# Optimization experiments

Measured on AMD Instinct MI355X. Metric: run time of the kernel, lower is better.

## Reference

```python
import jax, jax.numpy as jnp
import numpy as np

BATCH = 1024
N_KPS = 24
N_IN = 6
N_HID = 128
N_OUT = 2
N_EDGES = N_KPS * (N_KPS - 1)  # 552, fully-connected minus self-loops
BN_EPS = 1e-5


def _xavier(key, shape):
    # torch xavier_normal_: std = sqrt(2 / (fan_in + fan_out)); Linear weight is [out, in]
    std = np.sqrt(2.0 / (shape[0] + shape[1])).astype(np.float32)
    return jax.random.normal(key, shape, dtype=jnp.float32) * std


def _mlp(x, w1, b1, w2, b2, g, be):
    # Two-layer ELU MLP followed by training-mode BatchNorm1d over flattened (B*N, C)
    h = jax.nn.elu(jnp.einsum('bnd,hd->bnh', x, w1) + b1)
    h = jax.nn.elu(jnp.einsum('bnd,hd->bnh', h, w2) + b2)
    mean = h.mean(axis=(0, 1))
    var = h.var(axis=(0, 1))  # biased variance, as torch BN uses for normalization
    return g * (h - mean) * jax.lax.rsqrt(var + BN_EPS) + be


def setup_inputs() -> dict:
    key = jax.random.key(0)
    ks = jax.random.split(key, 12)
    # structural one-hot receiver/sender matrices for fully-connected graph (no self-loops)
    off = ~np.eye(N_KPS, dtype=bool)
    recv_idx, send_idx = np.nonzero(off)
    eye = np.eye(N_KPS, dtype=np.float32)
    rel_rec = jnp.asarray(eye[recv_idx])    # [E, N]
    rel_send = jnp.asarray(eye[send_idx])   # [E, N]

    inputs = jax.random.normal(ks[0], (BATCH, N_KPS, N_IN), dtype=jnp.float32)

    def mlp_params(k, n_in):
        k1, k2 = jax.random.split(k)
        return dict(
            w1=_xavier(k1, (N_HID, n_in)), b1=jnp.full((N_HID,), 0.1, jnp.float32),
            w2=_xavier(k2, (N_HID, N_HID)), b2=jnp.full((N_HID,), 0.1, jnp.float32),
            g=jnp.ones((N_HID,), jnp.float32), be=jnp.zeros((N_HID,), jnp.float32))

    m1 = mlp_params(ks[1], N_IN)
    m2 = mlp_params(ks[2], 2 * N_HID)
    m3 = mlp_params(ks[3], N_HID)
    m4 = mlp_params(ks[4], 3 * N_HID)
    fo_w = _xavier(ks[5], (N_OUT, N_HID * N_KPS))
    fo_b = jnp.full((N_OUT,), 0.1, jnp.float32)

    d = {'inputs': inputs, 'rel_rec': rel_rec, 'rel_send': rel_send,
         'fo_w': fo_w, 'fo_b': fo_b}
    for name, p in [('m1', m1), ('m2', m2), ('m3', m3), ('m4', m4)]:
        for k2, v in p.items():
            d[f'{name}_{k2}'] = v
    return d


def reference(inputs, rel_rec, rel_send,
              fo_w, fo_b,
              m1_w1, m1_b1, m1_w2, m1_b2, m1_g, m1_be,
              m2_w1, m2_b1, m2_w2, m2_b2, m2_g, m2_be,
              m3_w1, m3_b1, m3_w2, m3_b2, m3_g, m3_be,
              m4_w1, m4_b1, m4_w2, m4_b2, m4_g, m4_be):
    B, N = inputs.shape[0], inputs.shape[1]
    x = inputs.reshape(B, N, -1)

    def node2edge(x):  # [B,N,C] -> [B,E,2C]
        recv = jnp.einsum('en,bnc->bec', rel_rec, x)
        send = jnp.einsum('en,bnc->bec', rel_send, x)
        return jnp.concatenate([recv, send], axis=2)

    def edge2node(x):  # [B,E,C] -> [B,N,C], averaged by N (= incoming.size(1))
        return jnp.einsum('en,bec->bnc', rel_rec, x) / N

    x = _mlp(x, m1_w1, m1_b1, m1_w2, m1_b2, m1_g, m1_be)            # [B,N,H]
    x = _mlp(node2edge(x), m2_w1, m2_b1, m2_w2, m2_b2, m2_g, m2_be)  # [B,E,H]
    x_skip = x
    x = _mlp(edge2node(x), m3_w1, m3_b1, m3_w2, m3_b2, m3_g, m3_be)  # [B,N,H]
    x = node2edge(x)                                                  # [B,E,2H]
    x = jnp.concatenate([x, x_skip], axis=2)                          # [B,E,3H]
    x = _mlp(x, m4_w1, m4_b1, m4_w2, m4_b2, m4_g, m4_be)              # [B,E,H]
    x = edge2node(x)                                                  # [B,N,H]
    x = x.reshape(B, -1)                                              # [B,N*H]
    return x @ fo_w.T + fo_b                                          # [B,n_out]
```

## Files before the change

### kernel.cpp

```cpp
#include <hip/hip_runtime.h>

typedef __bf16 bf16;
typedef __bf16 b16x8 __attribute__((ext_vector_type(8)));
typedef __bf16 b16x4 __attribute__((ext_vector_type(4)));
typedef float f32x4 __attribute__((ext_vector_type(4)));

#define TB 256
#define LDA 136
#define NB 1024
#define NK 24
#define NE 552
#define NH 128
#define BEcnt (NB*NE)
#define BNODE (NB*NK)
#define EPS 1e-5f

#define S_BN1 0
#define S_BN3 2048
#define S_A2  4096
#define S_A4  20480
#define S_SC2 36864
#define S_SC4 37120
#define S_B41 37376
#define STATS_ZERO_BYTES 147456
#define WB_M1W2 0
#define WB_M2W1 16384
#define WB_M2W2 49152
#define WB_M3W1 65536
#define WB_M3W2 81920
#define WB_M4W1 98304
#define WB_M4W2 147456
#define WB_M4W1S 163840
#define OFF_WBF 150528ull
#define OFF_H1  516096ull
#define OFF_H3  (OFF_H1 + 6291456ull)
#define OFF_Y2R (OFF_H3 + 6291456ull)
#define OFF_Y2S (OFF_Y2R + 6291456ull)
#define OFF_Y4R (OFF_Y2S + 6291456ull)
#define OFF_Y4S (OFF_Y4R + 6291456ull)
#define OFF_Z2  (OFF_Y4S + 6291456ull)
#define OFF_Z4  (OFF_Z2  + 12582912ull)
#define OFF_H2  (OFF_Z4  + 12582912ull)

__device__ __forceinline__ float elu(float x){ return x > 0.f ? x : __expf(x) - 1.f; }

__device__ __forceinline__ void swizzle_bt(int id, int& b, int& tile4){
  int x = id & 7, j = id >> 3;
  int bt = j / 6;
  int tile = j - bt*6;
  b = x*128 + bt;
  tile4 = tile*4;
}

__device__ __forceinline__ void load_bfrags_bf(const bf16* W, int ldw, int k0,
                                               b16x8 bfr[4][2], int lane, int w){
  int n = lane & 15, q = lane >> 4;
  #pragma unroll
  for (int kb=0; kb<4; ++kb)
    #pragma unroll
    for (int t=0; t<2; ++t)
      bfr[kb][t] = *(const b16x8*)(W + (size_t)((w*2+t)*16 + n)*ldw + k0 + kb*32 + q*8);
}

template<int MT>
__device__ __forceinline__ void gemm_regB_t(const bf16* As, const b16x8 bfr[4][2],
                                            f32x4 acc[MT][2], int lane){
  int m = lane & 15, q = lane >> 4;
  #pragma unroll
  for (int kb=0; kb<4; ++kb){
    int ka = kb*32 + q*8;
    b16x8 a[MT];
    #pragma unroll
    for (int mt=0; mt<MT; ++mt)
      a[mt] = *(const b16x8*)(As + (mt*16+m)*LDA + ka);
    #pragma unroll
    for (int mt=0; mt<MT; ++mt)
      #pragma unroll
      for (int t=0; t<2; ++t)
        acc[mt][t] = __builtin_amdgcn_mfma_f32_16x16x32_bf16(a[mt], bfr[kb][t], acc[mt][t], 0,0,0);
  }
}

template<int MT>
__device__ __forceinline__ void zero_acc_t(f32x4 acc[MT][2]){
  #pragma unroll
  for (int mt=0; mt<MT; ++mt)
    #pragma unroll
    for (int t=0; t<2; ++t){ acc[mt][t][0]=0.f; acc[mt][t][1]=0.f; acc[mt][t][2]=0.f; acc[mt][t][3]=0.f; }
}

template<int MT>
__device__ __forceinline__ void epilogue_to_lds_t(const f32x4 acc[MT][2], const float* bias, bf16* As,
                                                  int lane, int w, int validRows){
  int q = lane >> 4, n = lane & 15;
  #pragma unroll
  for (int mt=0; mt<MT; ++mt)
    #pragma unroll
    for (int t=0; t<2; ++t){
      int col = (w*2+t)*16 + n;
      float bc = bias[col];
      #pragma unroll
      for (int i=0; i<4; ++i){
        int row = mt*16 + q*4 + i;
        float v = (row < validRows) ? elu(acc[mt][t][i] + bc) : 0.f;
        As[row*LDA + col] = (bf16)v;
      }
    }
}

template<int MT>
__device__ __forceinline__ void write_acc_bf_t(const f32x4 acc[MT][2], bf16* out, int lane, int w){
  int q = lane >> 4, n = lane & 15;
  #pragma unroll
  for (int mt=0; mt<MT; ++mt)
    #pragma unroll
    for (int t=0; t<2; ++t){
      int col = (w*2+t)*16 + n;
      #pragma unroll
      for (int i=0; i<4; ++i)
        out[(size_t)(mt*16 + q*4 + i)*NH + col] = (bf16)acc[mt][t][i];
    }
}

__device__ __forceinline__ void store_and_stats32(const bf16* As, bf16* g_out, float* bucket,
                                                  int tid){
  for (int i = tid; i < 32*16; i += TB){
    int row = i >> 4, c8 = (i & 15) << 3;
    *(b16x8*)(g_out + (size_t)row*NH + c8) = *(const b16x8*)(As + row*LDA + c8);
  }
  int c = tid & 127, half = tid >> 7;
  float s = 0.f, s2 = 0.f;
  for (int row = half; row < 32; row += 2){
    float v = (float)As[row*LDA + c];
    s += v; s2 += v*v;
  }
  atomicAdd(&bucket[c], s);
  atomicAdd(&bucket[128+c], s2);
}

__device__ __forceinline__ void build_A_g(bf16* As, const bf16* yrG, const bf16* ysG,
                                          const float* bias, int tile4, int tid){
  for (int i=tid; i<96*16; i+=TB){
    int row = i >> 4, c8 = (i & 15) << 3;
    b16x8 o;
    if (row < 92){
      int rl = (row>=23)+(row>=46)+(row>=69);
      int j = row - rl*23;
      int s = j + (j >= tile4 + rl);
      b16x8 vr = *(const b16x8*)(yrG + (size_t)rl*NH + c8);
      b16x8 vs = *(const b16x8*)(ysG + (size_t)s*NH + c8);
      #pragma unroll
      for (int k=0; k<8; ++k) o[k] = (bf16)elu((float)vr[k] + (float)vs[k] + bias[c8+k]);
    } else {
      #pragma unroll
      for (int k=0; k<8; ++k) o[k] = (bf16)0.f;
    }
    *(b16x8*)(As + row*LDA + c8) = o;
  }
}

__device__ __forceinline__ void harvest_core(const f32x4 acc[6][2], const float* bias, bf16* As,
                                             float* zL, float* sacc, int lane, int w){
  int q4 = (lane >> 4) << 2, n = lane & 15;
  int c0 = w*32 + n, c1 = c0 + 16;
  float b0 = bias[c0], b1 = bias[c1];
  float zs0[4] = {0,0,0,0}, zs1[4] = {0,0,0,0};
  float s0=0.f, p0=0.f, s1=0.f, p1=0.f;
  #pragma unroll
  for (int mt=0; mt<6; ++mt){
    #pragma unroll
    for (int i=0; i<4; ++i){
      const int R0 = mt*16 + i;
      int row = R0 + q4;
      bool ok = row < 92;
      float v0 = elu(acc[mt][0][i] + b0); v0 = ok ? v0 : 0.f;
      float v1 = elu(acc[mt][1][i] + b1); v1 = ok ? v1 : 0.f;
      if (As){
        As[row*LDA + c0] = (bf16)v0;
        As[row*LDA + c1] = (bf16)v1;
      }
      s0 += v0; p0 += v0*v0; s1 += v1; p1 += v1*v1;
      const int gLo = (R0>=23)+(R0>=46)+(R0>=69);
      const int gHi = ((R0+12)>=23)+((R0+12)>=46)+((R0+12)>=69);
      if (gLo == gHi){
        zs0[gLo] += v0; zs1[gLo] += v1;
      } else {
        const int bnd = (gHi==1) ? 23 : ((gHi==2) ? 46 : 69);
        bool hi = row >= bnd;
        zs0[gLo] += hi ? 0.f : v0;  zs0[gHi] += hi ? v0 : 0.f;
        zs1[gLo] += hi ? 0.f : v1;  zs1[gHi] += hi ? v1 : 0.f;
      }
    }
  }
  #pragma unroll
  for (int g=0; g<4; ++g){
    zs0[g] += __shfl_down(zs0[g],32); zs0[g] += __shfl_down(zs0[g],16);
    zs1[g] += __shfl_down(zs1[g],32); zs1[g] += __shfl_down(zs1[g],16);
  }
  s0 += __shfl_down(s0,32); s0 += __shfl_down(s0,16);
  p0 += __shfl_down(p0,32); p0 += __shfl_down(p0,16);
  s1 += __shfl_down(s1,32); s1 += __shfl_down(s1,16);
  p1 += __shfl_down(p1,32); p1 += __shfl_down(p1,16);
  if (lane < 16){
    #pragma unroll
    for (int g=0; g<4; ++g){
      zL[g*NH + c0] = zs0[g];
      zL[g*NH + c1] = zs1[g];
    }
    atomicAdd(&sacc[c0], s0);     atomicAdd(&sacc[128+c0], p0);
    atomicAdd(&sacc[c1], s1);     atomicAdd(&sacc[128+c1], p1);
  }
}

__global__ __launch_bounds__(TB) void k0_cvt(const float* __restrict__ s0, const float* __restrict__ s1,
    const float* __restrict__ s2, const float* __restrict__ s3, const float* __restrict__ s4,
    const float* __restrict__ s5, const float* __restrict__ s6, bf16* __restrict__ dst){
  int idx = (blockIdx.x*TB + threadIdx.x)*4;
  const float* sp; int base;
  if      (idx < 16384){ sp=s0; base=0; }
  else if (idx < 49152){ sp=s1; base=16384; }
  else if (idx < 65536){ sp=s2; base=49152; }
  else if (idx < 81920){ sp=s3; base=65536; }
  else if (idx < 98304){ sp=s4; base=81920; }
  else if (idx <147456){ sp=s5; base=98304; }
  else                 { sp=s6; base=147456; }
  f32x4 v = *(const f32x4*)(sp + (idx - base));
  b16x4 o; o[0]=(bf16)v[0]; o[1]=(bf16)v[1]; o[2]=(bf16)v[2]; o[3]=(bf16)v[3];
  *(b16x4*)(dst + idx) = o;
}

__global__ __launch_bounds__(TB) void k_fold41(const float* __restrict__ w41, const float* __restrict__ b41,
    const float* __restrict__ aff2, bf16* __restrict__ w41s, float* __restrict__ b41f){
  int tid = threadIdx.x;
  if (blockIdx.x < 16){
    int idx = (blockIdx.x*TB + tid)*4;
    int o = idx >> 7, k = idx & 127;
    f32x4 v = *(const f32x4*)(w41 + (size_t)o*384 + 256 + k);
    b16x4 r;
    #pragma unroll
    for (int j=0; j<4; ++j) r[j] = (bf16)(v[j] * aff2[k+j]);
    *(b16x4*)(w41s + idx) = r;
  } else if (tid < 128){
    const float* wr = w41 + (size_t)tid*384 + 256;
    float s = 0.f;
    for (int k=0; k<128; ++k) s += wr[k] * aff2[128+k];
    b41f[tid] = b41[tid] + s;
  }
}

__global__ __launch_bounds__(TB) void k1_mlp1(const float* __restrict__ in,
    const float* __restrict__ w1, const float* __restrict__ b1,
    const bf16* __restrict__ w2, const float* __restrict__ b2,
    bf16* __restrict__ h1, float* __restrict__ bn1){
  __shared__ alignas(16) bf16 As[32*LDA];
  __shared__ float w1s[128*6];
  __shared__ float b1s[128], b2s[128];
  __shared__ float ins[32*6];
  int tid = threadIdx.x;
  int row0 = blockIdx.x * 32;
  for (int i=tid; i<768; i+=TB) w1s[i] = w1[i];
  if (tid < 128){ b1s[tid]=b1[tid]; b2s[tid]=b2[tid]; }
  for (int i=tid; i<192; i+=TB) ins[i] = in[row0*6 + i];
  __syncthreads();
  for (int i=tid; i<32*32; i+=TB){
    int row = i >> 5, c4 = (i & 31) << 2;
    float x0=ins[row*6+0], x1=ins[row*6+1], x2=ins[row*6+2],
          x3=ins[row*6+3], x4=ins[row*6+4], x5=ins[row*6+5];
    #pragma unroll
    for (int j=0; j<4; ++j){
      int c = c4 + j;
      const float* wr = w1s + c*6;
      float s = b1s[c] + wr[0]*x0 + wr[1]*x1 + wr[2]*x2 + wr[3]*x3 + wr[4]*x4 + wr[5]*x5;
      As[row*LDA + c] = (bf16)elu(s);
    }
  }
  int lane = tid & 63, w = tid >> 6;
  b16x8 bfr[4][2];
  load_bfrags_bf(w2, 128, 0, bfr, lane, w);
  __syncthreads();
  f32x4 acc[2][2]; zero_acc_t<2>(acc);
  gemm_regB_t<2>(As, bfr, acc, lane);
  __syncthreads();
  epilogue_to_lds_t<2>(acc, b2s, As, lane, w, 32);
  __syncthreads();
  store_and_stats32(As, h1 + (size_t)row0*NH, bn1 + (blockIdx.x & 7)*256, tid);
}

__global__ __launch_bounds__(TB) void k_project(const bf16* __restrict__ hin,
    const float* __restrict__ stats,
    const float* __restrict__ g, const float* __restrict__ be,
    const bf16* __restrict__ Wp, int ldw,
    bf16* __restrict__ yr, bf16* __restrict__ ys){
  __shared__ alignas(16) bf16 As[32*LDA];
  __shared__ float scl[128], shf[128];
  int tid = threadIdx.x;
  int row0 = blockIdx.x * 32;
  if (tid < 128){
    float s = 0.f, q2 = 0.f;
    #pragma unroll
    for (int k=0; k<8; ++k){ s += stats[k*256+tid]; q2 += stats[k*256+128+tid]; }
    float mean = s / (float)BNODE;
    float var  = q2 / (float)BNODE - mean*mean;
    float rs = rsqrtf(var + EPS);
    float sc = g[tid] * rs;
    scl[tid] = sc; shf[tid] = be[tid] - mean*sc;
  }
  __syncthreads();
  for (int i=tid; i<32*16; i+=TB){
    int row = i >> 4, c8 = (i & 15) << 3;
    b16x8 v = *(const b16x8*)(hin + (size_t)(row0+row)*NH + c8);
    b16x8 o;
    #pragma unroll
    for (int j=0; j<8; ++j) o[j] = (bf16)(scl[c8+j]*(float)v[j] + shf[c8+j]);
    *(b16x8*)(As + row*LDA + c8) = o;
  }
  int lane = tid & 63, w = tid >> 6;
  b16x8 bfr[4][2];
  load_bfrags_bf(Wp, ldw, 0, bfr, lane, w);
  __syncthreads();
  f32x4 acc[2][2]; zero_acc_t<2>(acc);
  gemm_regB_t<2>(As, bfr, acc, lane);
  write_acc_bf_t<2>(acc, yr + (size_t)row0*NH, lane, w);
  load_bfrags_bf(Wp, ldw, 128, bfr, lane, w);
  zero_acc_t<2>(acc);
  gemm_regB_t<2>(As, bfr, acc, lane);
  write_acc_bf_t<2>(acc, ys + (size_t)row0*NH, lane, w);
}

__global__ __launch_bounds__(TB,4) void k3_edge1(const bf16* __restrict__ y2r, const bf16* __restrict__ y2s,
    const float* __restrict__ b21, const bf16* __restrict__ w22, const float* __restrict__ b22,
    float* __restrict__ z2, float* __restrict__ acc2, bf16* __restrict__ h2){
  __shared__ alignas(16) bf16 As[96*LDA];
  __shared__ float b1s[NH], b2s[NH];
  __shared__ float zL[512];
  int tid = threadIdx.x;
  int b, tile4; swizzle_bt(blockIdx.x, b, tile4);
  if (tid < NH){ b1s[tid]=b21[tid]; b2s[tid]=b22[tid]; }
  int lane = tid & 63, w = tid >> 6;
  b16x8 bfr[4][2];
  load_bfrags_bf(w22, 128, 0, bfr, lane, w);
  __syncthreads();
  build_A_g(As, y2r + ((size_t)b*NK + tile4)*NH, y2s + (size_t)b*NK*NH, b1s, tile4, tid);
  __syncthreads();
  f32x4 acc[6][2]; zero_acc_t<6>(acc);
  gemm_regB_t<6>(As, bfr, acc, lane);
  __syncthreads();
  harvest_core(acc, b2s, As, zL, acc2 + (blockIdx.x & 63)*256, lane, w);
  __syncthreads();
  float* zdst = z2 + (size_t)(b*NK + tile4)*NH;
  if (tid < 128) ((f32x4*)zdst)[tid] = ((const f32x4*)zL)[tid];
  bf16* h2g = h2 + ((size_t)b*NE + tile4*23)*NH;
  for (int i=tid; i<92*16; i+=TB){
    int row = i >> 4, c8 = (i & 15) << 3;
    *(b16x8*)(h2g + (size_t)row*NH + c8) = *(const b16x8*)(As + row*LDA + c8);
  }
}

__global__ __launch_bounds__(TB) void k_bnred(const float* __restrict__ A,
    const float* __restrict__ g, const float* __restrict__ be, float* __restrict__ aff){
  __shared__ float rs[256], rq[256];
  int tid = threadIdx.x;
  int col = blockIdx.x*16 + (tid & 15);
  int chunk = tid >> 4;
  float s=0.f, q=0.f;
  for (int r=0; r<4; ++r){
    int row = chunk*4 + r;
    s += A[row*256 + col];
    q += A[row*256 + 128 + col];
  }
  rs[tid]=s; rq[tid]=q;
  __syncthreads();
  if (tid < 16){
    float S=0.f, Q=0.f;
    #pragma unroll
    for (int c2=0; c2<16; ++c2){ S += rs[c2*16+tid]; Q += rq[c2*16+tid]; }
    int cc = blockIdx.x*16 + tid;
    float mean = S / (float)BEcnt;
    float var  = Q / (float)BEcnt - mean*mean;
    float sc = g[cc] * rsqrtf(var + EPS);
    aff[cc] = sc; aff[128+cc] = be[cc] - mean*sc;
  }
}

__global__ __launch_bounds__(TB) void k4a_mlp3(const float* __restrict__ z2,
    const float* __restrict__ aff2,
    const bf16* __restrict__ w31, const float* __restrict__ b31,
    const bf16* __restrict__ w32, const float* __restrict__ b32,
    bf16* __restrict__ h3, float* __restrict__ bn3){
  __shared__ alignas(16) bf16 As[32*LDA];
  __shared__ float scl[128], shf[128], b1s[128], b2s[128];
  int tid = threadIdx.x;
  int row0 = blockIdx.x * 32;
  if (tid < 128){
    scl[tid] = aff2[tid] * (1.f/24.f);
    shf[tid] = aff2[128+tid] * (23.f/24.f);
    b1s[tid] = b31[tid]; b2s[tid] = b32[tid];
  }
  __syncthreads();
  for (int i=tid; i<32*32; i+=TB){
    int rl = i >> 5, c4 = (i & 31) << 2;
    f32x4 v = *(const f32x4*)(z2 + (size_t)(row0+rl)*NH + c4);
    b16x4 o;
    #pragma unroll
    for (int k=0; k<4; ++k) o[k] = (bf16)(scl[c4+k]*v[k] + shf[c4+k]);
    *(b16x4*)(As + rl*LDA + c4) = o;
  }
  int lane = tid & 63, w = tid >> 6;
  b16x8 bfr[4][2];
  load_bfrags_bf(w31, 128, 0, bfr, lane, w);
  __syncthreads();
  f32x4 acc[2][2]; zero_acc_t<2>(acc);
  gemm_regB_t<2>(As, bfr, acc, lane);
  __syncthreads();
  epilogue_to_lds_t<2>(acc, b1s, As, lane, w, 32);
  load_bfrags_bf(w32, 128, 0, bfr, lane, w);
  __syncthreads();
  zero_acc_t<2>(acc);
  gemm_regB_t<2>(As, bfr, acc, lane);
  __syncthreads();
  epilogue_to_lds_t<2>(acc, b2s, As, lane, w, 32);
  __syncthreads();
  store_and_stats32(As, h3 + (size_t)row0*NH, bn3 + (blockIdx.x & 7)*256, tid);
}

__global__ __launch_bounds__(TB,3) void k5_edge2(
    const bf16* __restrict__ h2,
    const bf16* __restrict__ y4r, const bf16* __restrict__ y4s,
    const bf16* __restrict__ w41s, const float* __restrict__ b41f,
    const bf16* __restrict__ w42, const float* __restrict__ b42,
    float* __restrict__ z4, float* __restrict__ acc4){
  __shared__ alignas(16) bf16 As[96*LDA];
  __shared__ alignas(16) bf16 yt4[28*LDA];
  __shared__ float b41s[NH], b42s[NH];
  __shared__ float zL[512];
  int tid = threadIdx.x;
  int b, tile4; swizzle_bt(blockIdx.x, b, tile4);
  if (tid < NH){ b41s[tid]=b41f[tid]; b42s[tid]=b42[tid]; }
  int lane = tid & 63, w = tid >> 6;
  b16x8 bfr[4][2];
  load_bfrags_bf(w41s, 128, 0, bfr, lane, w);
  {
    const bf16* y4rG = y4r + ((size_t)b*NK + tile4)*NH;
    const bf16* y4sG = y4s + (size_t)b*NK*NH;
    for (int i=tid; i<448; i+=TB){
      int r = i >> 4, c8 = (i & 15) << 3;
      b16x8 v = (r < 4) ? *(const b16x8*)(y4rG + (size_t)r*NH + c8)
                        : *(const b16x8*)(y4sG + (size_t)(r-4)*NH + c8);
      *(b16x8*)(yt4 + r*LDA + c8) = v;
    }
  }
  {
    const bf16* h2g = h2 + ((size_t)b*NE + tile4*23)*NH;
    for (int i=tid; i<96*16; i+=TB){
      int row = i >> 4, c8 = (i & 15) << 3;
      b16x8 o;
      if (row < 92){
        o = *(const b16x8*)(h2g + (size_t)row*NH + c8);
      } else {
        #pragma unroll
        for (int j=0; j<8; ++j) o[j] = (bf16)0.f;
      }
      *(b16x8*)(As + row*LDA + c8) = o;
    }
  }
  __syncthreads();
  f32x4 acc[6][2]; zero_acc_t<6>(acc);
  gemm_regB_t<6>(As, bfr, acc, lane);
  load_bfrags_bf(w42, 128, 0, bfr, lane, w);
  __syncthreads();
  {
    int q = lane >> 4, n = lane & 15;
    #pragma unroll
    for (int mt=0; mt<6; ++mt)
      #pragma unroll
      for (int t=0; t<2; ++t){
        int col = w*32 + t*16 + n;
        #pragma unroll
        for (int i=0; i<4; ++i)
          As[(mt*16 + q*4 + i)*LDA + col] = (bf16)acc[mt][t][i];
      }
  }
  __syncthreads();
  for (int i=tid; i<96*16; i+=TB){
    int row = i >> 4, c8 = (i & 15) << 3;
    b16x8 o;
    if (row < 92){
      int rl = (row>=23)+(row>=46)+(row>=69);
      int j = row - rl*23;
      int s = j + (j >= tile4 + rl);
      b16x8 sk = *(const b16x8*)(As + row*LDA + c8);
      b16x8 vr = *(const b16x8*)(yt4 + rl*LDA + c8);
      b16x8 vs = *(const b16x8*)(yt4 + (4+s)*LDA + c8);
      #pragma unroll
      for (int k=0; k<8; ++k)
        o[k] = (bf16)elu((float)sk[k] + (float)vr[k] + (float)vs[k] + b41s[c8+k]);
    } else {
      #pragma unroll
      for (int k=0; k<8; ++k) o[k] = (bf16)0.f;
    }
    *(b16x8*)(As + row*LDA + c8) = o;
  }
  zero_acc_t<6>(acc);
  __syncthreads();
  gemm_regB_t<6>(As, bfr, acc, lane);
  harvest_core(acc, b42s, nullptr, zL, acc4 + (blockIdx.x & 63)*256, lane, w);
  __syncthreads();
  float* zdst = z4 + (size_t)(b*NK + tile4)*NH;
  if (tid < 128) ((f32x4*)zdst)[tid] = ((const f32x4*)zL)[tid];
}

__global__ __launch_bounds__(TB) void k6_out(const float* __restrict__ z4,
    const float* __restrict__ aff4,
    const float* __restrict__ fo_w, const float* __restrict__ fo_b, float* __restrict__ out){
  __shared__ float red[512];
  __shared__ float scl[128], shf[128];
  int tid = threadIdx.x, b = blockIdx.x;
  if (tid < 128){ scl[tid] = aff4[tid]; shf[tid] = aff4[128+tid]; }
  __syncthreads();
  const float inv24 = 1.f/24.f, f2324 = 23.f/24.f;
  float a0 = 0.f, a1 = 0.f;
  for (int i=tid; i<3072; i+=TB){
    int c = i & 127;
    float x = scl[c]*z4[(size_t)b*3072 + i]*inv24 + shf[c]*f2324;
    a0 += x * fo_w[i];
    a1 += x * fo_w[3072 + i];
  }
  red[tid] = a0; red[256+tid] = a1;
  __syncthreads();
  for (int st=128; st>0; st>>=1){
    if (tid < st){ red[tid] += red[tid+st]; red[256+tid] += red[256+tid+st]; }
    __syncthreads();
  }
  if (tid == 0){
    out[b*2+0] = red[0] + fo_b[0];
    out[b*2+1] = red[256] + fo_b[1];
  }
}

extern "C" void kernel_launch(void* const* d_in, const int* in_sizes, int n_in,
                              void* d_out, int out_size, void* d_ws, size_t ws_size,
                              hipStream_t stream){
  (void)in_sizes; (void)n_in; (void)out_size; (void)ws_size;
  const float* inputs = (const float*)d_in[0];
  const float* fo_w  = (const float*)d_in[3];
  const float* fo_b  = (const float*)d_in[4];
  const float* m1_w1=(const float*)d_in[5];  const float* m1_b1=(const float*)d_in[6];
  const float* m1_w2=(const float*)d_in[7];  const float* m1_b2=(const float*)d_in[8];
  const float* m1_g =(const float*)d_in[9];  const float* m1_be=(const float*)d_in[10];
  const float* m2_w1=(const float*)d_in[11]; const float* m2_b1=(const float*)d_in[12];
  const float* m2_w2=(const float*)d_in[13]; const float* m2_b2=(const float*)d_in[14];
  const float* m2_g =(const float*)d_in[15]; const float* m2_be=(const float*)d_in[16];
  const float* m3_w1=(const float*)d_in[17]; const float* m3_b1=(const float*)d_in[18];
  const float* m3_w2=(const float*)d_in[19]; const float* m3_b2=(const float*)d_in[20];
  const float* m3_g =(const float*)d_in[21]; const float* m3_be=(const float*)d_in[22];
  const float* m4_w1=(const float*)d_in[23]; const float* m4_b1=(const float*)d_in[24];
  const float* m4_w2=(const float*)d_in[25]; const float* m4_b2=(const float*)d_in[26];
  const float* m4_g =(const float*)d_in[27]; const float* m4_be=(const float*)d_in[28];

  char* ws = (char*)d_ws;
  float* stats = (float*)ws;
  bf16* wbf = (bf16*)(ws + OFF_WBF);
  bf16* h1  = (bf16*)(ws + OFF_H1);
  bf16* h3  = (bf16*)(ws + OFF_H3);
  bf16* y2r = (bf16*)(ws + OFF_Y2R);
  bf16* y2s = (bf16*)(ws + OFF_Y2S);
  bf16* y4r = (bf16*)(ws + OFF_Y4R);
  bf16* y4s = (bf16*)(ws + OFF_Y4S);
  float* z2  = (float*)(ws + OFF_Z2);
  float* z4  = (float*)(ws + OFF_Z4);
  bf16* h2  = (bf16*)(ws + OFF_H2);
  float* out = (float*)d_out;

  (void)hipMemsetAsync(d_ws, 0, STATS_ZERO_BYTES, stream);
  k0_cvt<<<160, TB, 0, stream>>>(m1_w2, m2_w1, m2_w2, m3_w1, m3_w2, m4_w1, m4_w2, wbf);
  k1_mlp1<<<768, TB, 0, stream>>>(inputs, m1_w1, m1_b1, wbf + WB_M1W2, m1_b2, h1, stats + S_BN1);
  k_project<<<768, TB, 0, stream>>>(h1, stats + S_BN1, m1_g, m1_be,
                                    wbf + WB_M2W1, 256, y2r, y2s);
  k3_edge1<<<6144, TB, 0, stream>>>(y2r, y2s, m2_b1, wbf + WB_M2W2, m2_b2, z2,
                                    stats + S_A2, h2);
  k_bnred<<<8, TB, 0, stream>>>(stats + S_A2, m2_g, m2_be, stats + S_SC2);
  k_fold41<<<17, TB, 0, stream>>>(m4_w1, m4_b1, stats + S_SC2, wbf + WB_M4W1S, stats + S_B41);
  k4a_mlp3<<<768, TB, 0, stream>>>(z2, stats + S_SC2, wbf + WB_M3W1, m3_b1,
                                   wbf + WB_M3W2, m3_b2, h3, stats + S_BN3);
  k_project<<<768, TB, 0, stream>>>(h3, stats + S_BN3, m3_g, m3_be,
                                    wbf + WB_M4W1, 384, y4r, y4s);
  k5_edge2<<<6144, TB, 0, stream>>>(h2, y4r, y4s,
                                    wbf + WB_M4W1S, stats + S_B41,
                                    wbf + WB_M4W2, m4_b2, z4, stats + S_A4);
  k_bnred<<<8, TB, 0, stream>>>(stats + S_A4, m4_g, m4_be, stats + S_SC4);
  k6_out<<<1024, TB, 0, stream>>>(z4, stats + S_SC4, fo_w, fo_b, out);
}
```

Before: 334.2 us.

## Fold BN reduction into consumers and add receiver/sender terms via augmented MFMA

Removes both k_bnred launches; each consumer kernel (k_fold41, k4a_mlp3, k6_out) now reduces the 64 partial BN stat rows itself and computes the scale and shift locally. In k5_edge2 the per-row addition of receiver, sender and bias projections is done by an extra 16x16x32 MFMA: a one-hot selector matrix is multiplied by a register fragment holding the y4r/y4s rows and the bias. This removes the separate LDS elementwise pass and one barrier, and ELU is applied when the accumulators are written out. The costs are redundant stat reductions in every block (768 and 1024 blocks each re-read 64x256 floats), scalar strided global loads to build the B fragments, and the bias being rounded to bf16.

After: 323.0 us. 1.03x faster.

```diff
diff --git a/kernel.cpp b/kernel.cpp
--- a/kernel.cpp
+++ b/kernel.cpp
@@ -7,6 +7,7 @@
 
 #define TB 256
 #define LDA 136
+#define LDI 40
 #define NB 1024
 #define NK 24
 #define NE 552
@@ -19,9 +20,7 @@
 #define S_BN3 2048
 #define S_A2  4096
 #define S_A4  20480
-#define S_SC2 36864
-#define S_SC4 37120
-#define S_B41 37376
+#define S_B41 36864
 #define STATS_ZERO_BYTES 147456
 #define WB_M1W2 0
 #define WB_M2W1 16384
@@ -230,20 +229,34 @@
 }
 
 __global__ __launch_bounds__(TB) void k_fold41(const float* __restrict__ w41, const float* __restrict__ b41,
-    const float* __restrict__ aff2, bf16* __restrict__ w41s, float* __restrict__ b41f){
+    const float* __restrict__ A2, const float* __restrict__ g2, const float* __restrict__ be2,
+    bf16* __restrict__ w41s, float* __restrict__ b41f){
+  __shared__ float tmp[256], scl[128], shf[128];
   int tid = threadIdx.x;
+  { int c = tid & 127, part = tid >> 7;
+    float s = 0.f;
+    for (int r=0; r<64; ++r) s += A2[r*256 + part*128 + c];
+    tmp[tid] = s; }
+  __syncthreads();
+  if (tid < 128){
+    float mean = tmp[tid] / (float)BEcnt;
+    float var  = tmp[128+tid] / (float)BEcnt - mean*mean;
+    float sc = g2[tid] * rsqrtf(var + EPS);
+    scl[tid] = sc; shf[tid] = be2[tid] - mean*sc;
+  }
+  __syncthreads();
   if (blockIdx.x < 16){
     int idx = (blockIdx.x*TB + tid)*4;
     int o = idx >> 7, k = idx & 127;
     f32x4 v = *(const f32x4*)(w41 + (size_t)o*384 + 256 + k);
     b16x4 r;
     #pragma unroll
-    for (int j=0; j<4; ++j) r[j] = (bf16)(v[j] * aff2[k+j]);
+    for (int j=0; j<4; ++j) r[j] = (bf16)(v[j] * scl[k+j]);
     *(b16x4*)(w41s + idx) = r;
   } else if (tid < 128){
     const float* wr = w41 + (size_t)tid*384 + 256;
     float s = 0.f;
-    for (int k=0; k<128; ++k) s += wr[k] * aff2[128+k];
+    for (int k=0; k<128; ++k) s += wr[k] * shf[k];
     b41f[tid] = b41[tid] + s;
   }
 }
@@ -356,45 +369,29 @@
   }
 }
 
-__global__ __launch_bounds__(TB) void k_bnred(const float* __restrict__ A,
-    const float* __restrict__ g, const float* __restrict__ be, float* __restrict__ aff){
-  __shared__ float rs[256], rq[256];
-  int tid = threadIdx.x;
-  int col = blockIdx.x*16 + (tid & 15);
-  int chunk = tid >> 4;
-  float s=0.f, q=0.f;
-  for (int r=0; r<4; ++r){
-    int row = chunk*4 + r;
-    s += A[row*256 + col];
-    q += A[row*256 + 128 + col];
-  }
-  rs[tid]=s; rq[tid]=q;
-  __syncthreads();
-  if (tid < 16){
-    float S=0.f, Q=0.f;
-    #pragma unroll
-    for (int c2=0; c2<16; ++c2){ S += rs[c2*16+tid]; Q += rq[c2*16+tid]; }
-    int cc = blockIdx.x*16 + tid;
-    float mean = S / (float)BEcnt;
-    float var  = Q / (float)BEcnt - mean*mean;
-    float sc = g[cc] * rsqrtf(var + EPS);
-    aff[cc] = sc; aff[128+cc] = be[cc] - mean*sc;
-  }
-}
-
 __global__ __launch_bounds__(TB) void k4a_mlp3(const float* __restrict__ z2,
-    const float* __restrict__ aff2,
+    const float* __restrict__ A2,
+    const float* __restrict__ g2, const float* __restrict__ be2,
     const bf16* __restrict__ w31, const float* __restrict__ b31,
     const bf16* __restrict__ w32, const float* __restrict__ b32,
     bf16* __restrict__ h3, float* __restrict__ bn3){
   __shared__ alignas(16) bf16 As[32*LDA];
   __shared__ float scl[128], shf[128], b1s[128], b2s[128];
+  __shared__ float tmp[256];
   int tid = threadIdx.x;
   int row0 = blockIdx.x * 32;
+  { int c = tid & 127, part = tid >> 7;
+    float s = 0.f;
+    for (int r=0; r<64; ++r) s += A2[r*256 + part*128 + c];
+    tmp[tid] = s; }
+  if (tid < 128){ b1s[tid] = b31[tid]; b2s[tid] = b32[tid]; }
+  __syncthreads();
   if (tid < 128){
-    scl[tid] = aff2[tid] * (1.f/24.f);
-    shf[tid] = aff2[128+tid] * (23.f/24.f);
-    b1s[tid] = b31[tid]; b2s[tid] = b32[tid];
+    float mean = tmp[tid] / (float)BEcnt;
+    float var  = tmp[128+tid] / (float)BEcnt - mean*mean;
+    float sc = g2[tid] * rsqrtf(var + EPS);
+    scl[tid] = sc * (1.f/24.f);
+    shf[tid] = (be2[tid] - mean*sc) * (23.f/24.f);
   }
   __syncthreads();
   for (int i=tid; i<32*32; i+=TB){
@@ -430,24 +427,48 @@
     const bf16* __restrict__ w42, const float* __restrict__ b42,
     float* __restrict__ z4, float* __restrict__ acc4){
   __shared__ alignas(16) bf16 As[96*LDA];
-  __shared__ alignas(16) bf16 yt4[28*LDA];
-  __shared__ float b41s[NH], b42s[NH];
+  __shared__ alignas(16) bf16 Ai[96*LDI];
+  __shared__ float b42s[NH];
   __shared__ float zL[512];
   int tid = threadIdx.x;
   int b, tile4; swizzle_bt(blockIdx.x, b, tile4);
-  if (tid < NH){ b41s[tid]=b41f[tid]; b42s[tid]=b42[tid]; }
+  if (tid < NH) b42s[tid] = b42[tid];
   int lane = tid & 63, w = tid >> 6;
   b16x8 bfr[4][2];
   load_bfrags_bf(w41s, 128, 0, bfr, lane, w);
+  b16x8 baug[2];
   {
     const bf16* y4rG = y4r + ((size_t)b*NK + tile4)*NH;
     const bf16* y4sG = y4s + (size_t)b*NK*NH;
-    for (int i=tid; i<448; i+=TB){
-      int r = i >> 4, c8 = (i & 15) << 3;
-      b16x8 v = (r < 4) ? *(const b16x8*)(y4rG + (size_t)r*NH + c8)
-                        : *(const b16x8*)(y4sG + (size_t)(r-4)*NH + c8);
-      *(b16x8*)(yt4 + r*LDA + c8) = v;
-    }
+    int q = lane >> 4, n = lane & 15;
+    #pragma unroll
+    for (int t=0; t<2; ++t){
+      int o = w*32 + t*16 + n;
+      #pragma unroll
+      for (int j=0; j<8; ++j){
+        int k = q*8 + j;
+        bf16 v;
+        if (k < 4)        v = y4rG[(size_t)k*NH + o];
+        else if (k < 28)  v = y4sG[(size_t)(k-4)*NH + o];
+        else if (k == 28) v = (bf16)b41f[o];
+        else              v = (bf16)0.f;
+        baug[t][j] = v;
+      }
+    }
+  }
+  for (int i=tid; i<96*4; i+=TB){
+    int row = i >> 2, cb = (i & 3) << 3;
+    int rl = (row>=23)+(row>=46)+(row>=69);
+    int jj = row - rl*23;
+    int s = jj + (jj >= tile4 + rl);
+    b16x8 o;
+    #pragma unroll
+    for (int k2=0; k2<8; ++k2){
+      int k = cb + k2;
+      bool one = (row < 92) && (k == rl || k == 4+s || k == 28);
+      o[k2] = one ? (bf16)1.f : (bf16)0.f;
+    }
+    *(b16x8*)(Ai + row*LDI + cb) = o;
   }
   {
     const bf16* h2g = h2 + ((size_t)b*NE + tile4*23)*NH;
@@ -466,6 +487,16 @@
   __syncthreads();
   f32x4 acc[6][2]; zero_acc_t<6>(acc);
   gemm_regB_t<6>(As, bfr, acc, lane);
+  {
+    int m = lane & 15, q = lane >> 4;
+    #pragma unroll
+    for (int mt=0; mt<6; ++mt){
+      b16x8 a = *(const b16x8*)(Ai + (mt*16+m)*LDI + q*8);
+      #pragma unroll
+      for (int t=0; t<2; ++t)
+        acc[mt][t] = __builtin_amdgcn_mfma_f32_16x16x32_bf16(a, baug[t], acc[mt][t], 0,0,0);
+    }
+  }
   load_bfrags_bf(w42, 128, 0, bfr, lane, w);
   __syncthreads();
   {
@@ -477,28 +508,8 @@
         int col = w*32 + t*16 + n;
         #pragma unroll
         for (int i=0; i<4; ++i)
-          As[(mt*16 + q*4 + i)*LDA + col] = (bf16)acc[mt][t][i];
+          As[(mt*16 + q*4 + i)*LDA + col] = (bf16)elu(acc[mt][t][i]);
       }
-  }
-  __syncthreads();
-  for (int i=tid; i<96*16; i+=TB){
-    int row = i >> 4, c8 = (i & 15) << 3;
-    b16x8 o;
-    if (row < 92){
-      int rl = (row>=23)+(row>=46)+(row>=69);
-      int j = row - rl*23;
-      int s = j + (j >= tile4 + rl);
-      b16x8 sk = *(const b16x8*)(As + row*LDA + c8);
-      b16x8 vr = *(const b16x8*)(yt4 + rl*LDA + c8);
-      b16x8 vs = *(const b16x8*)(yt4 + (4+s)*LDA + c8);
-      #pragma unroll
-      for (int k=0; k<8; ++k)
-        o[k] = (bf16)elu((float)sk[k] + (float)vr[k] + (float)vs[k] + b41s[c8+k]);
-    } else {
-      #pragma unroll
-      for (int k=0; k<8; ++k) o[k] = (bf16)0.f;
-    }
-    *(b16x8*)(As + row*LDA + c8) = o;
   }
   zero_acc_t<6>(acc);
   __syncthreads();
@@ -510,12 +521,23 @@
 }
 
 __global__ __launch_bounds__(TB) void k6_out(const float* __restrict__ z4,
-    const float* __restrict__ aff4,
+    const float* __restrict__ A4,
+    const float* __restrict__ g4, const float* __restrict__ be4,
     const float* __restrict__ fo_w, const float* __restrict__ fo_b, float* __restrict__ out){
   __shared__ float red[512];
   __shared__ float scl[128], shf[128];
   int tid = threadIdx.x, b = blockIdx.x;
-  if (tid < 128){ scl[tid] = aff4[tid]; shf[tid] = aff4[128+tid]; }
+  { int c = tid & 127, part = tid >> 7;
+    float s = 0.f;
+    for (int r=0; r<64; ++r) s += A4[r*256 + part*128 + c];
+    red[tid] = s; }
+  __syncthreads();
+  if (tid < 128){
+    float mean = red[tid] / (float)BEcnt;
+    float var  = red[128+tid] / (float)BEcnt - mean*mean;
+    float sc = g4[tid] * rsqrtf(var + EPS);
+    scl[tid] = sc; shf[tid] = be4[tid] - mean*sc;
+  }
   __syncthreads();
   const float inv24 = 1.f/24.f, f2324 = 23.f/24.f;
   float a0 = 0.f, a1 = 0.f;
@@ -525,6 +547,7 @@
     a0 += x * fo_w[i];
     a1 += x * fo_w[3072 + i];
   }
+  __syncthreads();
   red[tid] = a0; red[256+tid] = a1;
   __syncthreads();
   for (int st=128; st>0; st>>=1){
@@ -578,15 +601,15 @@
                                     wbf + WB_M2W1, 256, y2r, y2s);
   k3_edge1<<<6144, TB, 0, stream>>>(y2r, y2s, m2_b1, wbf + WB_M2W2, m2_b2, z2,
                                     stats + S_A2, h2);
-  k_bnred<<<8, TB, 0, stream>>>(stats + S_A2, m2_g, m2_be, stats + S_SC2);
-  k_fold41<<<17, TB, 0, stream>>>(m4_w1, m4_b1, stats + S_SC2, wbf + WB_M4W1S, stats + S_B41);
-  k4a_mlp3<<<768, TB, 0, stream>>>(z2, stats + S_SC2, wbf + WB_M3W1, m3_b1,
-                                   wbf + WB_M3W2, m3_b2, h3, stats + S_BN3);
+  k_fold41<<<17, TB, 0, stream>>>(m4_w1, m4_b1, stats + S_A2, m2_g, m2_be,
+                                  wbf + WB_M4W1S, stats + S_B41);
+  k4a_mlp3<<<768, TB, 0, stream>>>(z2, stats + S_A2, m2_g, m2_be,
+                                   wbf + WB_M3W1, m3_b1, wbf + WB_M3W2, m3_b2,
+                                   h3, stats + S_BN3);
   k_project<<<768, TB, 0, stream>>>(h3, stats + S_BN3, m3_g, m3_be,
                                     wbf + WB_M4W1, 384, y4r, y4s);
   k5_edge2<<<6144, TB, 0, stream>>>(h2, y4r, y4s,
                                     wbf + WB_M4W1S, stats + S_B41,
                                     wbf + WB_M4W2, m4_b2, z4, stats + S_A4);
-  k_bnred<<<8, TB, 0, stream>>>(stats + S_A4, m4_g, m4_be, stats + S_SC4);
-  k6_out<<<1024, TB, 0, stream>>>(z4, stats + S_SC4, fo_w, fo_b, out);
-}
+  k6_out<<<1024, TB, 0, stream>>>(z4, stats + S_A4, m4_g, m4_be, fo_w, fo_b, out);
+}
```
